# Kernel optimization log

Hardware: AMD Instinct MI355X
Metric: run time of the kernel (lower is better)

## Reference

```python
import jax, jax.numpy as jnp
import numpy as np

# NSAFlowLayer config (from init_kwargs)
W_ORTHO = 0.5      # w: blend weight of soft-polar retraction
MAX_ITER = 50      # max_iter (run fixed-length under jit; tol check omitted)
LR = 0.1           # 'default' initial learning rate for the fidelity gradient step
NS_ITERS = 8       # Newton-Schulz iterations for the (k,k) inverse matrix sqrt
EPS = 1e-8

B, P, K = 32, 16384, 64


def _invsqrt_ns(M):
    """Differentiable inverse sqrt of SPD (k,k) matrix via coupled Newton-Schulz."""
    k = M.shape[0]
    I = jnp.eye(k, dtype=M.dtype)
    nrm = jnp.trace(M) + EPS
    Y = M / nrm
    Z = I
    for _ in range(NS_ITERS):  # small fixed loop over k x k mats
        T = 0.5 * (3.0 * I - Z @ Y)
        Y = Y @ T
        Z = T @ Z
    return Z / jnp.sqrt(nrm)  # approx M^{-1/2}


def _nsa_flow_single(x0):
    """One independent NSA flow: gradient step on 0.5||Y-X0||^2, soft-polar
    retraction toward the Stiefel manifold, nonnegativity projection."""
    def step(Y, _):
        G = Y - x0                      # fidelity gradient (p,k)
        Y = Y - LR * G                  # gradient step
        S = _invsqrt_ns(Y.T @ Y)        # (k,k) inverse sqrt of Gram matrix
        Y = (1.0 - W_ORTHO) * Y + W_ORTHO * (Y @ S)  # soft polar retraction
        Y = jnp.maximum(Y, 0.0)         # nonneg projection
        return Y, None
    Yf, _ = jax.lax.scan(step, x0, None, length=MAX_ITER)  # Y0 = X0
    return Yf


def setup_inputs() -> dict:
    key = jax.random.key(0)
    X0 = jax.random.uniform(key, (B, P, K), dtype=jnp.float32)
    return {"X0": X0}


def reference(X0) -> jnp.ndarray:
    return jax.vmap(_nsa_flow_single)(X0)  # (B, p, k)
```

## Files before the change

kernel.cpp:

```cpp
#include <hip/hip_runtime.h>


#define BATCH 32
#define NP    16384
#define NK    64
#define NITER 50
#define NSIT  8
#define EPSC  1e-8f
#define CH    64
#define NT    256
#define NTNS  512
#define SP    68
#define SPH   72

using h4   = __attribute__((ext_vector_type(4))) _Float16;
using h8   = __attribute__((ext_vector_type(8))) _Float16;
using f32x4 = __attribute__((ext_vector_type(4))) float;

#define MFMA16x32(A, B, C) __builtin_amdgcn_mfma_f32_16x16x32_f16(A, B, C, 0, 0, 0)

#define FMA16(D, A0, A1, A2, A3, BV) do {                                  \
  D[0][0] = fmaf(A0, BV.x, D[0][0]); D[0][1] = fmaf(A0, BV.y, D[0][1]);    \
  D[0][2] = fmaf(A0, BV.z, D[0][2]); D[0][3] = fmaf(A0, BV.w, D[0][3]);    \
  D[1][0] = fmaf(A1, BV.x, D[1][0]); D[1][1] = fmaf(A1, BV.y, D[1][1]);    \
  D[1][2] = fmaf(A1, BV.z, D[1][2]); D[1][3] = fmaf(A1, BV.w, D[1][3]);    \
  D[2][0] = fmaf(A2, BV.x, D[2][0]); D[2][1] = fmaf(A2, BV.y, D[2][1]);    \
  D[2][2] = fmaf(A2, BV.z, D[2][2]); D[2][3] = fmaf(A2, BV.w, D[2][3]);    \
  D[3][0] = fmaf(A3, BV.x, D[3][0]); D[3][1] = fmaf(A3, BV.y, D[3][1]);    \
  D[3][2] = fmaf(A3, BV.z, D[3][2]); D[3][3] = fmaf(A3, BV.w, D[3][3]);    \
} while (0)

#define FMA8(D, A0, A1, BV) do {                                           \
  D[0][0] = fmaf(A0, BV.x, D[0][0]); D[0][1] = fmaf(A0, BV.y, D[0][1]);    \
  D[0][2] = fmaf(A0, BV.z, D[0][2]); D[0][3] = fmaf(A0, BV.w, D[0][3]);    \
  D[1][0] = fmaf(A1, BV.x, D[1][0]); D[1][1] = fmaf(A1, BV.y, D[1][1]);    \
  D[1][2] = fmaf(A1, BV.z, D[1][2]); D[1][3] = fmaf(A1, BV.w, D[1][3]);    \
} while (0)

__device__ __forceinline__ void gram_acc(const float (*sZ)[SP], int i0, int j0,
                                         float (&acc)[4][4]) {
#pragma unroll 8
  for (int r = 0; r < CH; ++r) {
    float4 zi = *(const float4*)&sZ[r][i0];
    float4 zj = *(const float4*)&sZ[r][j0];
    FMA16(acc, zi.x, zi.y, zi.z, zi.w, zj);
  }
}

__global__ __launch_bounds__(NT, 4) void k_init(const float* __restrict__ X0,
                                                float* __restrict__ Y,
                                                float* __restrict__ partials,
                                                int shift) {
  __shared__ float sZ[CH][SP];
  const int tid = threadIdx.x, blk = blockIdx.x;
  const int bpb = 1 << shift;
  const int b = blk >> shift, rb = blk & (bpb - 1);
  const int rpb = NP >> shift, nch = rpb / CH;
  const size_t base = ((size_t)b * NP + (size_t)rb * rpb) * NK;
  const float* __restrict__ x0 = X0 + base;
  float* __restrict__ y = Y + base;
  const int it = tid >> 4, jt = tid & 15;
  const int i0 = it * 4, j0 = jt * 4;
  float acc[4][4] = {{0.f}};

  for (int ch = 0; ch < nch; ++ch) {
    const float* xo = x0 + ch * CH * NK;
    float* yo = y + ch * CH * NK;
#pragma unroll
    for (int q = 0; q < 4; ++q) {
      int fi = (q * NT + tid) * 4;
      float4 xv = *(const float4*)(xo + fi);
      *(float4*)(yo + fi) = xv;
      int r = fi >> 6, c = fi & 63;
      *(float4*)&sZ[r][c] = xv;
    }
    __syncthreads();
    gram_acc(sZ, i0, j0, acc);
    __syncthreads();
  }
  float* p = partials + (size_t)blk * NK * NK;
#pragma unroll
  for (int a = 0; a < 4; ++a)
    *(float4*)(p + (i0 + a) * NK + j0) =
        make_float4(acc[a][0], acc[a][1], acc[a][2], acc[a][3]);
}

__global__ __launch_bounds__(NTNS, 2) void k_ns(const float* __restrict__ partials,
                                                _Float16* __restrict__ Sthi,
                                                _Float16* __restrict__ Stlo,
                                                int npart) {
  __shared__ float sA[NK][SP];
  __shared__ float sB[NK][SP];
  __shared__ float sT[NK][SP];
  __shared__ float sRed[8];

  const int tid = threadIdx.x, b = blockIdx.x;
  const int it = tid >> 4, jt = tid & 15;
  const int i0 = it * 2, j0 = jt * 4;

  float m[2][4] = {{0.f}};
  const float* pb = partials + (size_t)b * npart * NK * NK;
#pragma unroll 4
  for (int p = 0; p < npart; ++p) {
    const float* pp = pb + (size_t)p * NK * NK;
#pragma unroll
    for (int a = 0; a < 2; ++a) {
      float4 v = *(const float4*)(pp + (i0 + a) * NK + j0);
      m[a][0] += v.x; m[a][1] += v.y; m[a][2] += v.z; m[a][3] += v.w;
    }
  }
  float local = 0.f;
#pragma unroll
  for (int a = 0; a < 2; ++a)
#pragma unroll
    for (int c = 0; c < 4; ++c)
      if ((i0 + a) == (j0 + c)) local += m[a][c];
#pragma unroll
  for (int off = 32; off; off >>= 1) local += __shfl_down(local, off);
  if ((tid & 63) == 0) sRed[tid >> 6] = local;
  __syncthreads();
  float nrm = EPSC;
#pragma unroll
  for (int w = 0; w < 8; ++w) nrm += sRed[w];
  const float inv = 1.0f / nrm;

#pragma unroll
  for (int a = 0; a < 2; ++a)
#pragma unroll
    for (int c = 0; c < 4; ++c) {
      sA[i0 + a][j0 + c] = m[a][c] * inv;
      sB[i0 + a][j0 + c] = (i0 + a) == (j0 + c) ? 1.0f : 0.0f;
    }
  __syncthreads();

  {
#pragma unroll
    for (int a = 0; a < 2; ++a)
#pragma unroll
      for (int c = 0; c < 4; ++c)
        sT[i0 + a][j0 + c] =
            (((i0 + a) == (j0 + c)) ? 1.5f : 0.0f) - 0.5f * sA[i0 + a][j0 + c];
    __syncthreads();
    float r1[2][4] = {{0.f}};
#pragma unroll 8
    for (int k = 0; k < NK; ++k) {
      float y0 = sA[i0 + 0][k], y1 = sA[i0 + 1][k];
      float4 tv = *(const float4*)&sT[k][j0];
      FMA8(r1, y0, y1, tv);
    }
    __syncthreads();
#pragma unroll
    for (int a = 0; a < 2; ++a)
#pragma unroll
      for (int c = 0; c < 4; ++c) {
        sA[i0 + a][j0 + c] = r1[a][c];
        sB[i0 + a][j0 + c] = sT[i0 + a][j0 + c];
      }
    __syncthreads();
  }

  for (int ns = 1; ns < NSIT; ++ns) {
    float d[2][4] = {{0.f}};
#pragma unroll 8
    for (int k = 0; k < NK; ++k) {
      float b0 = sB[i0 + 0][k], b1 = sB[i0 + 1][k];
      float4 av = *(const float4*)&sA[k][j0];
      FMA8(d, b0, b1, av);
    }
#pragma unroll
    for (int a = 0; a < 2; ++a)
#pragma unroll
      for (int c = 0; c < 4; ++c)
        sT[i0 + a][j0 + c] =
            (((i0 + a) == (j0 + c)) ? 1.5f : 0.0f) - 0.5f * d[a][c];
    __syncthreads();

    float r1[2][4] = {{0.f}}, r2[2][4] = {{0.f}};
#pragma unroll 8
    for (int k = 0; k < NK; ++k) {
      float y0 = sA[i0 + 0][k], y1 = sA[i0 + 1][k];
      float4 tv = *(const float4*)&sT[k][j0];
      FMA8(r1, y0, y1, tv);
      float t0 = sT[i0 + 0][k], t1 = sT[i0 + 1][k];
      float4 zv = *(const float4*)&sB[k][j0];
      FMA8(r2, t0, t1, zv);
    }
    __syncthreads();
#pragma unroll
    for (int a = 0; a < 2; ++a)
#pragma unroll
      for (int c = 0; c < 4; ++c) {
        sA[i0 + a][j0 + c] = r1[a][c];
        sB[i0 + a][j0 + c] = r2[a][c];
      }
    __syncthreads();
  }

  const float sc = 1.0f / sqrtf(nrm);
  _Float16* Sh = Sthi + (size_t)b * NK * NK;
  _Float16* Sl = Stlo + (size_t)b * NK * NK;
#pragma unroll
  for (int a = 0; a < 2; ++a)
#pragma unroll
    for (int c = 0; c < 4; ++c) {
      float s = sB[i0 + a][j0 + c] * sc;
      _Float16 hh = (_Float16)s;
      Sh[(j0 + c) * NK + (i0 + a)] = hh;
      Sl[(j0 + c) * NK + (i0 + a)] = (_Float16)((s - (float)hh) * 2048.f);
    }
}

__global__ __launch_bounds__(NT, 4) void k_fused(
    const float* __restrict__ X0, float* __restrict__ Y,
    const _Float16* __restrict__ Sthi, const _Float16* __restrict__ Stlo,
    float* __restrict__ partials, int last, int shift) {
  __shared__ _Float16 sYa[CH][SPH];
  __shared__ _Float16 sYb[CH][SPH];
  __shared__ _Float16 sSa[NK][SPH];
  __shared__ _Float16 sSb[NK][SPH];

  const int tid = threadIdx.x, blk = blockIdx.x;
  const int bpb = 1 << shift;
  const int b = blk >> shift, rb = blk & (bpb - 1);
  const int rpb = NP >> shift, nch = rpb / CH;
  const size_t base = ((size_t)b * NP + (size_t)rb * rpb) * NK;
  const float* __restrict__ x0 = X0 + base;
  float* __restrict__ y = Y + base;

  {
    const _Float16* sh = Sthi + (size_t)b * NK * NK;
    const _Float16* sl = Stlo + (size_t)b * NK * NK;
    int r = tid >> 2, c = (tid & 3) * 16;
    const uint4* gh = (const uint4*)(sh + r * NK + c);
    const uint4* gl = (const uint4*)(sl + r * NK + c);
    uint4* dh = (uint4*)&sSa[r][c];
    uint4* dl = (uint4*)&sSb[r][c];
    dh[0] = gh[0]; dh[1] = gh[1];
    dl[0] = gl[0]; dl[1] = gl[1];
  }

  const int wv = tid >> 6, ln = tid & 63;
  const int lr = ln & 15, lq = ln >> 4;

  f32x4 gacc[4], glo[4];
#pragma unroll
  for (int t = 0; t < 4; ++t) {
    gacc[t] = (f32x4){0.f, 0.f, 0.f, 0.f};
    glo[t]  = (f32x4){0.f, 0.f, 0.f, 0.f};
  }
  __syncthreads();

  for (int ch = 0; ch < nch; ++ch) {
    const float* xo = x0 + ch * CH * NK;
    float* yo = y + ch * CH * NK;

#pragma unroll
    for (int q = 0; q < 4; ++q) {
      int fi = (q * NT + tid) * 4;
      int r = fi >> 6, c = fi & 63;
      float4 yv = *(const float4*)(yo + fi);
      float4 xv = *(const float4*)(xo + fi);
      float p0 = fmaf(0.9f, yv.x, 0.1f * xv.x);
      float p1 = fmaf(0.9f, yv.y, 0.1f * xv.y);
      float p2 = fmaf(0.9f, yv.z, 0.1f * xv.z);
      float p3 = fmaf(0.9f, yv.w, 0.1f * xv.w);
      _Float16 h0 = (_Float16)p0, h1 = (_Float16)p1;
      _Float16 h2 = (_Float16)p2, h3 = (_Float16)p3;
      *(h4*)&sYa[r][c] = (h4){h0, h1, h2, h3};
      *(h4*)&sYb[r][c] = (h4){(_Float16)((p0 - (float)h0) * 2048.f),
                              (_Float16)((p1 - (float)h1) * 2048.f),
                              (_Float16)((p2 - (float)h2) * 2048.f),
                              (_Float16)((p3 - (float)h3) * 2048.f)};
    }
    __syncthreads();

    h8 a_hi[2], a_lo[2];
#pragma unroll
    for (int kh = 0; kh < 2; ++kh) {
      a_hi[kh] = *(const h8*)&sYa[16 * wv + lr][lq * 8 + 32 * kh];
      a_lo[kh] = *(const h8*)&sYb[16 * wv + lr][lq * 8 + 32 * kh];
    }
    f32x4 dot[4];
    float ypv[4][4];
#pragma unroll
    for (int tc = 0; tc < 4; ++tc) {
      f32x4 ah = (f32x4){0.f, 0.f, 0.f, 0.f};
      f32x4 al = (f32x4){0.f, 0.f, 0.f, 0.f};
#pragma unroll
      for (int kh = 0; kh < 2; ++kh) {
        h8 b_hi = *(const h8*)&sSa[16 * tc + lr][lq * 8 + 32 * kh];
        h8 b_lo = *(const h8*)&sSb[16 * tc + lr][lq * 8 + 32 * kh];
        ah = MFMA16x32(a_hi[kh], b_hi, ah);
        al = MFMA16x32(a_hi[kh], b_lo, al);
        al = MFMA16x32(a_lo[kh], b_hi, al);
      }
      dot[tc] = ah + al * (1.f / 2048.f);
#pragma unroll
      for (int r_ = 0; r_ < 4; ++r_) {
        int R = 16 * wv + 4 * lq + r_, C = 16 * tc + lr;
        ypv[tc][r_] = (float)sYa[R][C] + (float)sYb[R][C] * (1.f / 2048.f);
      }
    }
    __syncthreads();

#pragma unroll
    for (int tc = 0; tc < 4; ++tc) {
#pragma unroll
      for (int r_ = 0; r_ < 4; ++r_) {
        int R = 16 * wv + 4 * lq + r_, C = 16 * tc + lr;
        float yn = fmaxf(0.5f * ypv[tc][r_] + 0.5f * dot[tc][r_], 0.f);
        yo[R * NK + C] = yn;
        if (!last) {
          float z = fmaf(0.9f, yn, 0.1f * xo[R * NK + C]);
          _Float16 zh = (_Float16)z;
          sYa[C][R] = zh;
          sYb[C][R] = (_Float16)((z - (float)zh) * 2048.f);
        }
      }
    }
    __syncthreads();

    if (!last) {
      h8 ga_hi[2], ga_lo[2];
#pragma unroll
      for (int kh = 0; kh < 2; ++kh) {
        ga_hi[kh] = *(const h8*)&sYa[16 * wv + lr][lq * 8 + 32 * kh];
        ga_lo[kh] = *(const h8*)&sYb[16 * wv + lr][lq * 8 + 32 * kh];
      }
#pragma unroll
      for (int tc = 0; tc < 4; ++tc) {
        f32x4 lt = (f32x4){0.f, 0.f, 0.f, 0.f};
#pragma unroll
        for (int kh = 0; kh < 2; ++kh) {
          h8 gb_hi = *(const h8*)&sYa[16 * tc + lr][lq * 8 + 32 * kh];
          h8 gb_lo = *(const h8*)&sYb[16 * tc + lr][lq * 8 + 32 * kh];
          gacc[tc] = MFMA16x32(ga_hi[kh], gb_hi, gacc[tc]);
          lt = MFMA16x32(ga_hi[kh], gb_lo, lt);
          lt = MFMA16x32(ga_lo[kh], gb_hi, lt);
        }
        glo[tc] += lt;
      }
    }
    __syncthreads();
  }

  if (!last) {
    float* p = partials + (size_t)blk * NK * NK;
#pragma unroll
    for (int tc = 0; tc < 4; ++tc)
#pragma unroll
      for (int r_ = 0; r_ < 4; ++r_) {
        int R = 16 * wv + 4 * lq + r_, C = 16 * tc + lr;
        p[R * NK + C] = gacc[tc][r_] + glo[tc][r_] * (1.f / 2048.f);
      }
  }
}

extern "C" void kernel_launch(void* const* d_in, const int* in_sizes, int n_in,
                              void* d_out, int out_size, void* d_ws,
                              size_t ws_size, hipStream_t stream) {
  (void)in_sizes; (void)n_in; (void)out_size;
  const float* X0 = (const float*)d_in[0];
  float* Y = (float*)d_out;

  const size_t slotf = (size_t)NK * NK;
  const size_t need5 = ((size_t)(BATCH << 5)) * slotf * 4
                       + 2 * (size_t)BATCH * slotf * 2;
  const int shift = (ws_size >= need5) ? 5 : 4;
  const int nblk = BATCH << shift;

  float* partials = (float*)d_ws;
  _Float16* Sthi = (_Float16*)((char*)d_ws + (size_t)nblk * slotf * 4);
  _Float16* Stlo = Sthi + (size_t)BATCH * slotf;

  k_init<<<nblk, NT, 0, stream>>>(X0, Y, partials, shift);
  for (int t = 0; t < NITER; ++t) {
    k_ns<<<BATCH, NTNS, 0, stream>>>(partials, Sthi, Stlo, 1 << shift);
    k_fused<<<nblk, NT, 0, stream>>>(X0, Y, Sthi, Stlo, partials,
                                     t == NITER - 1 ? 1 : 0, shift);
  }
}
```

Before: 8.595 ms.

## Fuse Newton-Schulz solve into tail block of fused kernel via atomic counter

Removes the separate per-iteration Newton-Schulz kernel: the last block finishing each batch (found with an atomic counter and threadfence) reduces the partial Gram matrices and computes the inverse square root inline, so the next fused launch can start without an extra small launch. It also folds the 0.5 blend into S (S' = 0.5 I + 0.5 S), so the retraction becomes one matmul, and keeps the S fragments in registers instead of shared memory. Shared memory is reused through a union and occupancy drops to 3 blocks per unit. The tail-block solve runs serially at the end of each launch with only 256 threads, which may lengthen that kernel's critical path.

```diff
diff --git a/kernel.cpp b/kernel.cpp
--- a/kernel.cpp
+++ b/kernel.cpp
@@ -9,12 +9,11 @@
 #define EPSC  1e-8f
 #define CH    64
 #define NT    256
-#define NTNS  512
 #define SP    68
 #define SPH   72
 
-using h4   = __attribute__((ext_vector_type(4))) _Float16;
-using h8   = __attribute__((ext_vector_type(8))) _Float16;
+using h4    = __attribute__((ext_vector_type(4))) _Float16;
+using h8    = __attribute__((ext_vector_type(8))) _Float16;
 using f32x4 = __attribute__((ext_vector_type(4))) float;
 
 #define MFMA16x32(A, B, C) __builtin_amdgcn_mfma_f32_16x16x32_f16(A, B, C, 0, 0, 0)
@@ -30,29 +29,135 @@
   D[3][2] = fmaf(A3, BV.z, D[3][2]); D[3][3] = fmaf(A3, BV.w, D[3][3]);    \
 } while (0)
 
-#define FMA8(D, A0, A1, BV) do {                                           \
-  D[0][0] = fmaf(A0, BV.x, D[0][0]); D[0][1] = fmaf(A0, BV.y, D[0][1]);    \
-  D[0][2] = fmaf(A0, BV.z, D[0][2]); D[0][3] = fmaf(A0, BV.w, D[0][3]);    \
-  D[1][0] = fmaf(A1, BV.x, D[1][0]); D[1][1] = fmaf(A1, BV.y, D[1][1]);    \
-  D[1][2] = fmaf(A1, BV.z, D[1][2]); D[1][3] = fmaf(A1, BV.w, D[1][3]);    \
-} while (0)
-
-__device__ __forceinline__ void gram_acc(const float (*sZ)[SP], int i0, int j0,
-                                         float (&acc)[4][4]) {
+union SMemF {
+  struct { _Float16 a[CH][SPH]; _Float16 b[CH][SPH]; } zt;
+  struct { float Y[NK][SP]; float Z[NK][SP]; float T[NK][SP];
+           float red[16]; int tail; } ns;
+};
+
+__device__ void ns_compute(SMemF& sm, const float* __restrict__ pb, int npart,
+                           _Float16* __restrict__ S2h,
+                           _Float16* __restrict__ S2l, int tid) {
+  float (*sA)[SP] = sm.ns.Y;
+  float (*sB)[SP] = sm.ns.Z;
+  float (*sT)[SP] = sm.ns.T;
+  const int it = tid >> 4, jt = tid & 15;
+  const int i0 = it * 4, j0 = jt * 4;
+
+  float m[4][4] = {{0.f}};
+  for (int p = 0; p < npart; ++p) {
+    const float* pp = pb + (size_t)p * NK * NK;
+#pragma unroll
+    for (int a = 0; a < 4; ++a) {
+      float4 v = *(const float4*)(pp + (i0 + a) * NK + j0);
+      m[a][0] += v.x; m[a][1] += v.y; m[a][2] += v.z; m[a][3] += v.w;
+    }
+  }
+  if (it == jt) sm.ns.red[it] = m[0][0] + m[1][1] + m[2][2] + m[3][3];
+  __syncthreads();
+  float nrm = EPSC;
+#pragma unroll
+  for (int i = 0; i < 16; ++i) nrm += sm.ns.red[i];
+  const float inv = 1.0f / nrm;
+
+#pragma unroll
+  for (int a = 0; a < 4; ++a)
+#pragma unroll
+    for (int c = 0; c < 4; ++c)
+      sA[i0 + a][j0 + c] = m[a][c] * inv;
+  __syncthreads();
+
+  {
+    float t[4][4];
+#pragma unroll
+    for (int a = 0; a < 4; ++a)
+#pragma unroll
+      for (int c = 0; c < 4; ++c) {
+        t[a][c] = (((i0 + a) == (j0 + c)) ? 1.5f : 0.0f) -
+                  0.5f * sA[i0 + a][j0 + c];
+        sT[i0 + a][j0 + c] = t[a][c];
+      }
+    __syncthreads();
+    float r1[4][4] = {{0.f}};
 #pragma unroll 8
-  for (int r = 0; r < CH; ++r) {
-    float4 zi = *(const float4*)&sZ[r][i0];
-    float4 zj = *(const float4*)&sZ[r][j0];
-    FMA16(acc, zi.x, zi.y, zi.z, zi.w, zj);
-  }
+    for (int k = 0; k < NK; ++k) {
+      float y0 = sA[i0 + 0][k], y1 = sA[i0 + 1][k];
+      float y2 = sA[i0 + 2][k], y3 = sA[i0 + 3][k];
+      float4 tv = *(const float4*)&sT[k][j0];
+      FMA16(r1, y0, y1, y2, y3, tv);
+    }
+    __syncthreads();
+#pragma unroll
+    for (int a = 0; a < 4; ++a)
+#pragma unroll
+      for (int c = 0; c < 4; ++c) {
+        sA[i0 + a][j0 + c] = r1[a][c];
+        sB[i0 + a][j0 + c] = t[a][c];
+      }
+    __syncthreads();
+  }
+
+  for (int ns = 1; ns < NSIT; ++ns) {
+    float d[4][4] = {{0.f}};
+#pragma unroll 8
+    for (int k = 0; k < NK; ++k) {
+      float b0 = sB[i0 + 0][k], b1 = sB[i0 + 1][k];
+      float b2 = sB[i0 + 2][k], b3 = sB[i0 + 3][k];
+      float4 av = *(const float4*)&sA[k][j0];
+      FMA16(d, b0, b1, b2, b3, av);
+    }
+#pragma unroll
+    for (int a = 0; a < 4; ++a)
+#pragma unroll
+      for (int c = 0; c < 4; ++c)
+        sT[i0 + a][j0 + c] =
+            (((i0 + a) == (j0 + c)) ? 1.5f : 0.0f) - 0.5f * d[a][c];
+    __syncthreads();
+
+    float r1[4][4] = {{0.f}}, r2[4][4] = {{0.f}};
+#pragma unroll 8
+    for (int k = 0; k < NK; ++k) {
+      float y0 = sA[i0 + 0][k], y1 = sA[i0 + 1][k];
+      float y2 = sA[i0 + 2][k], y3 = sA[i0 + 3][k];
+      float4 tv = *(const float4*)&sT[k][j0];
+      FMA16(r1, y0, y1, y2, y3, tv);
+      float t0 = sT[i0 + 0][k], t1 = sT[i0 + 1][k];
+      float t2 = sT[i0 + 2][k], t3 = sT[i0 + 3][k];
+      float4 zv = *(const float4*)&sB[k][j0];
+      FMA16(r2, t0, t1, t2, t3, zv);
+    }
+    __syncthreads();
+#pragma unroll
+    for (int a = 0; a < 4; ++a)
+#pragma unroll
+      for (int c = 0; c < 4; ++c) {
+        sA[i0 + a][j0 + c] = r1[a][c];
+        sB[i0 + a][j0 + c] = r2[a][c];
+      }
+    __syncthreads();
+  }
+
+  const float sc = 0.5f / sqrtf(nrm);
+#pragma unroll
+  for (int a = 0; a < 4; ++a)
+#pragma unroll
+    for (int c = 0; c < 4; ++c) {
+      float s = sB[i0 + a][j0 + c] * sc +
+                (((i0 + a) == (j0 + c)) ? 0.5f : 0.0f);
+      _Float16 hh = (_Float16)s;
+      S2h[(i0 + a) * NK + (j0 + c)] = hh;
+      S2l[(i0 + a) * NK + (j0 + c)] = (_Float16)((s - (float)hh) * 2048.f);
+    }
 }
 
 __global__ __launch_bounds__(NT, 4) void k_init(const float* __restrict__ X0,
                                                 float* __restrict__ Y,
                                                 float* __restrict__ partials,
+                                                unsigned* __restrict__ cnt,
                                                 int shift) {
   __shared__ float sZ[CH][SP];
   const int tid = threadIdx.x, blk = blockIdx.x;
+  if (blk == 0 && tid < BATCH) cnt[tid] = 0u;
   const int bpb = 1 << shift;
   const int b = blk >> shift, rb = blk & (bpb - 1);
   const int rpb = NP >> shift, nch = rpb / CH;
@@ -75,7 +180,12 @@
       *(float4*)&sZ[r][c] = xv;
     }
     __syncthreads();
-    gram_acc(sZ, i0, j0, acc);
+#pragma unroll 8
+    for (int r = 0; r < CH; ++r) {
+      float4 zi = *(const float4*)&sZ[r][i0];
+      float4 zj = *(const float4*)&sZ[r][j0];
+      FMA16(acc, zi.x, zi.y, zi.z, zi.w, zj);
+    }
     __syncthreads();
   }
   float* p = partials + (size_t)blk * NK * NK;
@@ -85,139 +195,22 @@
         make_float4(acc[a][0], acc[a][1], acc[a][2], acc[a][3]);
 }
 
-__global__ __launch_bounds__(NTNS, 2) void k_ns(const float* __restrict__ partials,
-                                                _Float16* __restrict__ Sthi,
-                                                _Float16* __restrict__ Stlo,
-                                                int npart) {
-  __shared__ float sA[NK][SP];
-  __shared__ float sB[NK][SP];
-  __shared__ float sT[NK][SP];
-  __shared__ float sRed[8];
-
-  const int tid = threadIdx.x, b = blockIdx.x;
-  const int it = tid >> 4, jt = tid & 15;
-  const int i0 = it * 2, j0 = jt * 4;
-
-  float m[2][4] = {{0.f}};
-  const float* pb = partials + (size_t)b * npart * NK * NK;
-#pragma unroll 4
-  for (int p = 0; p < npart; ++p) {
-    const float* pp = pb + (size_t)p * NK * NK;
-#pragma unroll
-    for (int a = 0; a < 2; ++a) {
-      float4 v = *(const float4*)(pp + (i0 + a) * NK + j0);
-      m[a][0] += v.x; m[a][1] += v.y; m[a][2] += v.z; m[a][3] += v.w;
-    }
-  }
-  float local = 0.f;
-#pragma unroll
-  for (int a = 0; a < 2; ++a)
-#pragma unroll
-    for (int c = 0; c < 4; ++c)
-      if ((i0 + a) == (j0 + c)) local += m[a][c];
-#pragma unroll
-  for (int off = 32; off; off >>= 1) local += __shfl_down(local, off);
-  if ((tid & 63) == 0) sRed[tid >> 6] = local;
-  __syncthreads();
-  float nrm = EPSC;
-#pragma unroll
-  for (int w = 0; w < 8; ++w) nrm += sRed[w];
-  const float inv = 1.0f / nrm;
-
-#pragma unroll
-  for (int a = 0; a < 2; ++a)
-#pragma unroll
-    for (int c = 0; c < 4; ++c) {
-      sA[i0 + a][j0 + c] = m[a][c] * inv;
-      sB[i0 + a][j0 + c] = (i0 + a) == (j0 + c) ? 1.0f : 0.0f;
-    }
-  __syncthreads();
-
-  {
-#pragma unroll
-    for (int a = 0; a < 2; ++a)
-#pragma unroll
-      for (int c = 0; c < 4; ++c)
-        sT[i0 + a][j0 + c] =
-            (((i0 + a) == (j0 + c)) ? 1.5f : 0.0f) - 0.5f * sA[i0 + a][j0 + c];
-    __syncthreads();
-    float r1[2][4] = {{0.f}};
-#pragma unroll 8
-    for (int k = 0; k < NK; ++k) {
-      float y0 = sA[i0 + 0][k], y1 = sA[i0 + 1][k];
-      float4 tv = *(const float4*)&sT[k][j0];
-      FMA8(r1, y0, y1, tv);
-    }
-    __syncthreads();
-#pragma unroll
-    for (int a = 0; a < 2; ++a)
-#pragma unroll
-      for (int c = 0; c < 4; ++c) {
-        sA[i0 + a][j0 + c] = r1[a][c];
-        sB[i0 + a][j0 + c] = sT[i0 + a][j0 + c];
-      }
-    __syncthreads();
-  }
-
-  for (int ns = 1; ns < NSIT; ++ns) {
-    float d[2][4] = {{0.f}};
-#pragma unroll 8
-    for (int k = 0; k < NK; ++k) {
-      float b0 = sB[i0 + 0][k], b1 = sB[i0 + 1][k];
-      float4 av = *(const float4*)&sA[k][j0];
-      FMA8(d, b0, b1, av);
-    }
-#pragma unroll
-    for (int a = 0; a < 2; ++a)
-#pragma unroll
-      for (int c = 0; c < 4; ++c)
-        sT[i0 + a][j0 + c] =
-            (((i0 + a) == (j0 + c)) ? 1.5f : 0.0f) - 0.5f * d[a][c];
-    __syncthreads();
-
-    float r1[2][4] = {{0.f}}, r2[2][4] = {{0.f}};
-#pragma unroll 8
-    for (int k = 0; k < NK; ++k) {
-      float y0 = sA[i0 + 0][k], y1 = sA[i0 + 1][k];
-      float4 tv = *(const float4*)&sT[k][j0];
-      FMA8(r1, y0, y1, tv);
-      float t0 = sT[i0 + 0][k], t1 = sT[i0 + 1][k];
-      float4 zv = *(const float4*)&sB[k][j0];
-      FMA8(r2, t0, t1, zv);
-    }
-    __syncthreads();
-#pragma unroll
-    for (int a = 0; a < 2; ++a)
-#pragma unroll
-      for (int c = 0; c < 4; ++c) {
-        sA[i0 + a][j0 + c] = r1[a][c];
-        sB[i0 + a][j0 + c] = r2[a][c];
-      }
-    __syncthreads();
-  }
-
-  const float sc = 1.0f / sqrtf(nrm);
-  _Float16* Sh = Sthi + (size_t)b * NK * NK;
-  _Float16* Sl = Stlo + (size_t)b * NK * NK;
-#pragma unroll
-  for (int a = 0; a < 2; ++a)
-#pragma unroll
-    for (int c = 0; c < 4; ++c) {
-      float s = sB[i0 + a][j0 + c] * sc;
-      _Float16 hh = (_Float16)s;
-      Sh[(j0 + c) * NK + (i0 + a)] = hh;
-      Sl[(j0 + c) * NK + (i0 + a)] = (_Float16)((s - (float)hh) * 2048.f);
-    }
-}
-
-__global__ __launch_bounds__(NT, 4) void k_fused(
+__global__ __launch_bounds__(NT, 3) void k_ns_once(
+    const float* __restrict__ partials, _Float16* __restrict__ S2h,
+    _Float16* __restrict__ S2l, int bpb) {
+  __shared__ SMemF sm;
+  const int b = blockIdx.x;
+  ns_compute(sm, partials + (size_t)b * bpb * NK * NK, bpb,
+             S2h + (size_t)b * NK * NK, S2l + (size_t)b * NK * NK,
+             threadIdx.x);
+}
+
+__global__ __launch_bounds__(NT, 3) void k_fused(
     const float* __restrict__ X0, float* __restrict__ Y,
-    const _Float16* __restrict__ Sthi, const _Float16* __restrict__ Stlo,
-    float* __restrict__ partials, int last, int shift) {
-  __shared__ _Float16 sYa[CH][SPH];
-  __shared__ _Float16 sYb[CH][SPH];
-  __shared__ _Float16 sSa[NK][SPH];
-  __shared__ _Float16 sSb[NK][SPH];
+    const _Float16* __restrict__ S2h, const _Float16* __restrict__ S2l,
+    float* __restrict__ partials, unsigned* __restrict__ cnt,
+    int last, int shift) {
+  __shared__ SMemF sm;
 
   const int tid = threadIdx.x, blk = blockIdx.x;
   const int bpb = 1 << shift;
@@ -227,20 +220,22 @@
   const float* __restrict__ x0 = X0 + base;
   float* __restrict__ y = Y + base;
 
-  {
-    const _Float16* sh = Sthi + (size_t)b * NK * NK;
-    const _Float16* sl = Stlo + (size_t)b * NK * NK;
-    int r = tid >> 2, c = (tid & 3) * 16;
-    const uint4* gh = (const uint4*)(sh + r * NK + c);
-    const uint4* gl = (const uint4*)(sl + r * NK + c);
-    uint4* dh = (uint4*)&sSa[r][c];
-    uint4* dl = (uint4*)&sSb[r][c];
-    dh[0] = gh[0]; dh[1] = gh[1];
-    dl[0] = gl[0]; dl[1] = gl[1];
-  }
-
   const int wv = tid >> 6, ln = tid & 63;
   const int lr = ln & 15, lq = ln >> 4;
+
+  h8 sb_h[4][2], sb_l[4][2];
+  {
+    const _Float16* s2h = S2h + (size_t)b * NK * NK;
+    const _Float16* s2l = S2l + (size_t)b * NK * NK;
+#pragma unroll
+    for (int tc = 0; tc < 4; ++tc)
+#pragma unroll
+      for (int kh = 0; kh < 2; ++kh) {
+        int off = (16 * tc + lr) * NK + 32 * kh + 8 * lq;
+        sb_h[tc][kh] = *(const h8*)(s2h + off);
+        sb_l[tc][kh] = *(const h8*)(s2l + off);
+      }
+  }
 
   f32x4 gacc[4], glo[4];
 #pragma unroll
@@ -248,7 +243,6 @@
     gacc[t] = (f32x4){0.f, 0.f, 0.f, 0.f};
     glo[t]  = (f32x4){0.f, 0.f, 0.f, 0.f};
   }
-  __syncthreads();
 
   for (int ch = 0; ch < nch; ++ch) {
     const float* xo = x0 + ch * CH * NK;
@@ -266,77 +260,77 @@
       float p3 = fmaf(0.9f, yv.w, 0.1f * xv.w);
       _Float16 h0 = (_Float16)p0, h1 = (_Float16)p1;
       _Float16 h2 = (_Float16)p2, h3 = (_Float16)p3;
-      *(h4*)&sYa[r][c] = (h4){h0, h1, h2, h3};
-      *(h4*)&sYb[r][c] = (h4){(_Float16)((p0 - (float)h0) * 2048.f),
-                              (_Float16)((p1 - (float)h1) * 2048.f),
-                              (_Float16)((p2 - (float)h2) * 2048.f),
-                              (_Float16)((p3 - (float)h3) * 2048.f)};
-    }
-    __syncthreads();
-
-    h8 a_hi[2], a_lo[2];
+      *(h4*)&sm.zt.a[r][c] = (h4){h0, h1, h2, h3};
+      *(h4*)&sm.zt.b[r][c] = (h4){(_Float16)((p0 - (float)h0) * 2048.f),
+                                  (_Float16)((p1 - (float)h1) * 2048.f),
+                                  (_Float16)((p2 - (float)h2) * 2048.f),
+                                  (_Float16)((p3 - (float)h3) * 2048.f)};
+    }
+    __syncthreads();
+
+    h8 a_h[2], a_l[2];
 #pragma unroll
     for (int kh = 0; kh < 2; ++kh) {
-      a_hi[kh] = *(const h8*)&sYa[16 * wv + lr][lq * 8 + 32 * kh];
-      a_lo[kh] = *(const h8*)&sYb[16 * wv + lr][lq * 8 + 32 * kh];
+      a_h[kh] = *(const h8*)&sm.zt.a[16 * wv + lr][8 * lq + 32 * kh];
+      a_l[kh] = *(const h8*)&sm.zt.b[16 * wv + lr][8 * lq + 32 * kh];
     }
     f32x4 dot[4];
-    float ypv[4][4];
 #pragma unroll
     for (int tc = 0; tc < 4; ++tc) {
       f32x4 ah = (f32x4){0.f, 0.f, 0.f, 0.f};
       f32x4 al = (f32x4){0.f, 0.f, 0.f, 0.f};
 #pragma unroll
       for (int kh = 0; kh < 2; ++kh) {
-        h8 b_hi = *(const h8*)&sSa[16 * tc + lr][lq * 8 + 32 * kh];
-        h8 b_lo = *(const h8*)&sSb[16 * tc + lr][lq * 8 + 32 * kh];
-        ah = MFMA16x32(a_hi[kh], b_hi, ah);
-        al = MFMA16x32(a_hi[kh], b_lo, al);
-        al = MFMA16x32(a_lo[kh], b_hi, al);
+        ah = MFMA16x32(a_h[kh], sb_h[tc][kh], ah);
+        al = MFMA16x32(a_h[kh], sb_l[tc][kh], al);
+        al = MFMA16x32(a_l[kh], sb_h[tc][kh], al);
       }
       dot[tc] = ah + al * (1.f / 2048.f);
+    }
+    __syncthreads();
+
+    const int R0 = 16 * wv + 4 * lq;
+#pragma unroll
+    for (int tc = 0; tc < 4; ++tc) {
+      const int C = 16 * tc + lr;
+      float yn[4];
 #pragma unroll
       for (int r_ = 0; r_ < 4; ++r_) {
-        int R = 16 * wv + 4 * lq + r_, C = 16 * tc + lr;
-        ypv[tc][r_] = (float)sYa[R][C] + (float)sYb[R][C] * (1.f / 2048.f);
-      }
-    }
-    __syncthreads();
-
-#pragma unroll
-    for (int tc = 0; tc < 4; ++tc) {
-#pragma unroll
-      for (int r_ = 0; r_ < 4; ++r_) {
-        int R = 16 * wv + 4 * lq + r_, C = 16 * tc + lr;
-        float yn = fmaxf(0.5f * ypv[tc][r_] + 0.5f * dot[tc][r_], 0.f);
-        yo[R * NK + C] = yn;
-        if (!last) {
-          float z = fmaf(0.9f, yn, 0.1f * xo[R * NK + C]);
-          _Float16 zh = (_Float16)z;
-          sYa[C][R] = zh;
-          sYb[C][R] = (_Float16)((z - (float)zh) * 2048.f);
+        yn[r_] = fmaxf(dot[tc][r_], 0.f);
+        yo[(R0 + r_) * NK + C] = yn[r_];
+      }
+      if (!last) {
+        h4 zh, zl;
+#pragma unroll
+        for (int r_ = 0; r_ < 4; ++r_) {
+          float z = fmaf(0.9f, yn[r_], 0.1f * xo[(R0 + r_) * NK + C]);
+          _Float16 hh = (_Float16)z;
+          zh[r_] = hh;
+          zl[r_] = (_Float16)((z - (float)hh) * 2048.f);
         }
+        *(h4*)&sm.zt.a[C][R0] = zh;
+        *(h4*)&sm.zt.b[C][R0] = zl;
       }
     }
     __syncthreads();
 
     if (!last) {
-      h8 ga_hi[2], ga_lo[2];
+      h8 ga_h[2], ga_l[2];
 #pragma unroll
       for (int kh = 0; kh < 2; ++kh) {
-        ga_hi[kh] = *(const h8*)&sYa[16 * wv + lr][lq * 8 + 32 * kh];
-        ga_lo[kh] = *(const h8*)&sYb[16 * wv + lr][lq * 8 + 32 * kh];
+        ga_h[kh] = *(const h8*)&sm.zt.a[16 * wv + lr][8 * lq + 32 * kh];
+        ga_l[kh] = *(const h8*)&sm.zt.b[16 * wv + lr][8 * lq + 32 * kh];
       }
 #pragma unroll
       for (int tc = 0; tc < 4; ++tc) {
         f32x4 lt = (f32x4){0.f, 0.f, 0.f, 0.f};
 #pragma unroll
         for (int kh = 0; kh < 2; ++kh) {
-          h8 gb_hi = *(const h8*)&sYa[16 * tc + lr][lq * 8 + 32 * kh];
-          h8 gb_lo = *(const h8*)&sYb[16 * tc + lr][lq * 8 + 32 * kh];
-          gacc[tc] = MFMA16x32(ga_hi[kh], gb_hi, gacc[tc]);
-          lt = MFMA16x32(ga_hi[kh], gb_lo, lt);
-          lt = MFMA16x32(ga_lo[kh], gb_hi, lt);
+          h8 gb_h = *(const h8*)&sm.zt.a[16 * tc + lr][8 * lq + 32 * kh];
+          h8 gb_l = *(const h8*)&sm.zt.b[16 * tc + lr][8 * lq + 32 * kh];
+          gacc[tc] = MFMA16x32(ga_h[kh], gb_h, gacc[tc]);
+          lt = MFMA16x32(ga_h[kh], gb_l, lt);
+          lt = MFMA16x32(ga_l[kh], gb_h, lt);
         }
         glo[tc] += lt;
       }
@@ -346,13 +340,30 @@
 
   if (!last) {
     float* p = partials + (size_t)blk * NK * NK;
-#pragma unroll
-    for (int tc = 0; tc < 4; ++tc)
-#pragma unroll
-      for (int r_ = 0; r_ < 4; ++r_) {
-        int R = 16 * wv + 4 * lq + r_, C = 16 * tc + lr;
-        p[R * NK + C] = gacc[tc][r_] + glo[tc][r_] * (1.f / 2048.f);
-      }
+    const int R0 = 16 * wv + 4 * lq;
+#pragma unroll
+    for (int tc = 0; tc < 4; ++tc) {
+      const int C = 16 * tc + lr;
+      float4 g = make_float4(gacc[tc][0] + glo[tc][0] * (1.f / 2048.f),
+                             gacc[tc][1] + glo[tc][1] * (1.f / 2048.f),
+                             gacc[tc][2] + glo[tc][2] * (1.f / 2048.f),
+                             gacc[tc][3] + glo[tc][3] * (1.f / 2048.f));
+      *(float4*)(p + C * NK + R0) = g;
+    }
+    __syncthreads();
+
+    if (tid == 0) {
+      __threadfence();
+      unsigned old = atomicAdd(&cnt[b], 1u);
+      sm.ns.tail = (((old + 1) & (unsigned)(bpb - 1)) == 0u) ? 1 : 0;
+    }
+    __syncthreads();
+    if (sm.ns.tail) {
+      __threadfence();
+      ns_compute(sm, partials + (size_t)b * bpb * NK * NK, bpb,
+                 (_Float16*)S2h + (size_t)b * NK * NK,
+                 (_Float16*)S2l + (size_t)b * NK * NK, tid);
+    }
   }
 }
 
@@ -365,18 +376,20 @@
 
   const size_t slotf = (size_t)NK * NK;
   const size_t need5 = ((size_t)(BATCH << 5)) * slotf * 4
-                       + 2 * (size_t)BATCH * slotf * 2;
+                       + 2 * (size_t)BATCH * slotf * 2
+                       + BATCH * sizeof(unsigned);
   const int shift = (ws_size >= need5) ? 5 : 4;
   const int nblk = BATCH << shift;
 
   float* partials = (float*)d_ws;
-  _Float16* Sthi = (_Float16*)((char*)d_ws + (size_t)nblk * slotf * 4);
-  _Float16* Stlo = Sthi + (size_t)BATCH * slotf;
-
-  k_init<<<nblk, NT, 0, stream>>>(X0, Y, partials, shift);
+  _Float16* S2h = (_Float16*)((char*)d_ws + (size_t)nblk * slotf * 4);
+  _Float16* S2l = S2h + (size_t)BATCH * slotf;
+  unsigned* cnt = (unsigned*)(S2l + (size_t)BATCH * slotf);
+
+  k_init<<<nblk, NT, 0, stream>>>(X0, Y, partials, cnt, shift);
+  k_ns_once<<<BATCH, NT, 0, stream>>>(partials, S2h, S2l, 1 << shift);
   for (int t = 0; t < NITER; ++t) {
-    k_ns<<<BATCH, NTNS, 0, stream>>>(partials, Sthi, Stlo, 1 << shift);
-    k_fused<<<nblk, NT, 0, stream>>>(X0, Y, Sthi, Stlo, partials,
+    k_fused<<<nblk, NT, 0, stream>>>(X0, Y, S2h, S2l, partials, cnt,
                                      t == NITER - 1 ? 1 : 0, shift);
   }
 }
```

Measured after the change: 18.09 ms. +110.4%, slower.
